# Performance work log

Hardware: AMD Instinct MI355X
Metric: run time of the kernel (lower is better)

Reference implementation:

```python
import jax, jax.numpy as jnp
import numpy as np
from jax import lax

G = 64; ELL = 0.18; VOX = ELL / G
C_VIEWS = 6; H_IMG = 256; W_IMG = 256
MAX_N = 2048; PT = 0.25; MT = 0.25; FILL = 0.45
CHUNK = 256; RADIUS_CLIP = 2.0; NEAR = 0.01


def _rotz(a):
    c, s = jnp.cos(a), jnp.sin(a)
    z = jnp.zeros_like(c); o = jnp.ones_like(c)
    return jnp.stack([jnp.stack([c, -s, z]), jnp.stack([s, c, z]), jnp.stack([z, z, o])])


def _quat_to_mat4(q):
    # faithful replication of quaternion_matrix_torch_batch (incl. its asymmetries), fp32
    eps = 4 * np.finfo(np.float32).eps
    n = jnp.sum(q * q, 1)
    qs = q * jnp.sqrt(2.0 / jnp.where(n < eps, 1.0, n))[:, None]
    o = jnp.einsum('bi,bj->bij', qs, qs)
    one = jnp.ones_like(n); zero = jnp.zeros_like(n)
    row0 = jnp.stack([1.0 - o[:, 2, 2] - o[:, 3, 3], o[:, 1, 2] - o[:, 3, 0], o[:, 1, 3] + o[:, 2, 0], zero], 1)
    row1 = jnp.stack([o[:, 1, 2] - o[:, 3, 0], one, o[:, 2, 3] - o[:, 1, 0], zero], 1)
    row2 = jnp.stack([o[:, 1, 3] - o[:, 2, 0], o[:, 2, 3] + o[:, 1, 0], 1.0 - o[:, 1, 1] - o[:, 2, 2], zero], 1)
    row3 = jnp.stack([zero, zero, zero, one], 1)
    M = jnp.stack([row0, row1, row2, row3], 1)
    return jnp.where((n < eps)[:, None, None], jnp.eye(4, dtype=q.dtype), M)


def _quat_from_mat4(m):
    m00, m01, m02 = m[:, 0, 0], m[:, 0, 1], m[:, 0, 2]
    m10, m11, m12 = m[:, 1, 0], m[:, 1, 1], m[:, 1, 2]
    m20, m21, m22 = m[:, 2, 0], m[:, 2, 1], m[:, 2, 2]
    r0 = jnp.stack([m00 - m11 - m22, m01 + m10, m02 + m20, m21 - m12], 1)
    r1 = jnp.stack([m01 + m10, m11 - m00 - m22, m12 + m21, m02 - m20], 1)
    r2 = jnp.stack([m02 + m20, m12 + m21, m22 - m00 - m11, m10 - m01], 1)
    r3 = jnp.stack([m21 - m12, m02 - m20, m10 - m01, m00 + m11 + m22], 1)
    K = jnp.stack([r0, r1, r2, r3], 1) / 3.0
    _, V = jnp.linalg.eigh(K)
    q = V[:, :, -1][:, jnp.array([3, 0, 1, 2])]
    return jnp.where(q[:, :1] < 0.0, -q, q)


def _splat(means, quats, scales, opac, colors, viewmat, K, bg):
    R3, t3 = viewmat[:3, :3], viewmat[:3, 3]
    cam = means @ R3.T + t3
    x, y, z = cam[:, 0], cam[:, 1], cam[:, 2]
    fx, fy, cx, cy = K[0, 0], K[1, 1], K[0, 2], K[1, 2]
    qn = quats / (jnp.linalg.norm(quats, axis=1, keepdims=True) + 1e-12)
    w, qx, qy, qz = qn[:, 0], qn[:, 1], qn[:, 2], qn[:, 3]
    Rq = jnp.stack([
        jnp.stack([1 - 2 * (qy * qy + qz * qz), 2 * (qx * qy - w * qz), 2 * (qx * qz + w * qy)], 1),
        jnp.stack([2 * (qx * qy + w * qz), 1 - 2 * (qx * qx + qz * qz), 2 * (qy * qz - w * qx)], 1),
        jnp.stack([2 * (qx * qz - w * qy), 2 * (qy * qz + w * qx), 1 - 2 * (qx * qx + qy * qy)], 1)], 1)
    cov3 = jnp.einsum('nij,nj,nkj->nik', Rq, scales ** 2, Rq)
    covc = jnp.einsum('ij,njk,lk->nil', R3, cov3, R3)
    rz = 1.0 / z
    zn = jnp.zeros_like(z)
    J = jnp.stack([jnp.stack([fx * rz, zn, -fx * x * rz * rz], 1),
                   jnp.stack([zn, fy * rz, -fy * y * rz * rz], 1)], 1)  # [N,2,3]
    cov2 = jnp.einsum('nij,njk,nlk->nil', J, covc, J)
    a2 = cov2[:, 0, 0] + 0.3; b2 = cov2[:, 0, 1]; c2 = cov2[:, 1, 1] + 0.3  # gsplat screen dilation
    det = a2 * c2 - b2 * b2
    det_s = jnp.where(det > 1e-12, det, 1.0)
    ca = c2 / det_s; cb = -b2 / det_s; cc = a2 / det_s  # conic
    lam = 0.5 * (a2 + c2) + jnp.sqrt(jnp.maximum(0.25 * (a2 - c2) ** 2 + b2 * b2, 1e-12))
    radius = jnp.ceil(3.0 * jnp.sqrt(lam))
    mu_x = fx * x * rz + cx; mu_y = fy * y * rz + cy
    valid = (z > NEAR) & (det > 1e-12) & (radius > RADIUS_CLIP)
    op = jnp.where(valid, opac, 0.0)
    order = jnp.argsort(z)  # front-to-back
    gac = lambda a: a[order].reshape(-1, CHUNK, *a.shape[1:])
    chunks = (gac(mu_x), gac(mu_y), gac(ca), gac(cb), gac(cc), gac(op), gac(colors))
    xs = jnp.arange(W_IMG, dtype=means.dtype) + 0.5
    ys = jnp.arange(H_IMG, dtype=means.dtype) + 0.5

    @jax.checkpoint
    def body(carry, ch):
        rgb, T = carry
        ux, uy, A, B, Cc, o_, col = ch
        dx = xs[None, None, :] - ux[:, None, None]          # [c,1,W]->[c,H,W]
        dy = ys[None, :, None] - uy[:, None, None]
        sigma = 0.5 * (A[:, None, None] * dx * dx + Cc[:, None, None] * dy * dy) + B[:, None, None] * dx * dy
        alpha = o_[:, None, None] * jnp.exp(-sigma)
        alpha = jnp.where((sigma >= 0) & (alpha >= 1.0 / 255.0), jnp.minimum(alpha, 0.999), 0.0)
        cp = jnp.cumprod(1.0 - alpha, axis=0)
        Tin = jnp.concatenate([jnp.ones_like(cp[:1]), cp[:-1]], 0)  # exclusive transmittance in chunk
        wgt = alpha * Tin * T[None]
        rgb = rgb + jnp.einsum('nhw,nc->hwc', wgt, col)
        return (rgb, T * cp[-1]), None

    init = (jnp.zeros((H_IMG, W_IMG, 3), means.dtype), jnp.ones((H_IMG, W_IMG), means.dtype))
    (rgb, T), _ = lax.scan(body, init, chunks)
    alpha_img = 1.0 - T
    rgb = jnp.clip(rgb + T[..., None] * bg, 0.0, 1.0)
    return rgb[None], alpha_img[None, :, :, None]


def _forward(mask, img, p_3d, angle, grid, Ks, viewmats, w1, b1, w2, b2, scale_param, background, view_num):
    m = mask[0]; im = img[0]
    Rz = _rotz(angle)
    # ---- shape carving: project canonical grid into all views ----
    pw = grid @ Rz.T + p_3d                                   # [V,3]
    cam = jnp.einsum('cij,vj->cvi', viewmats[:, :3, :3], pw) + viewmats[:, None, :3, 3]
    z = cam[..., 2]
    proj = jnp.einsum('cij,cvj->cvi', Ks, cam)
    u = proj[..., 0] / z; v = proj[..., 1] / z
    ui = jnp.clip(jnp.round(u).astype(jnp.int32), 0, W_IMG - 1)
    vi = jnp.clip(jnp.round(v).astype(jnp.int32), 0, H_IMG - 1)
    inb = (u >= 0) & (u < W_IMG) & (v >= 0) & (v < H_IMG) & (z > NEAR)
    cidx = jnp.arange(C_VIEWS)[:, None]
    inside = inb & (m[cidx, vi, ui] > 0.5)
    csamp = im[cidx, vi, ui]                                  # [C,V,3]
    wv = inside.astype(grid.dtype)
    frac = wv.mean(0)
    col = (wv[..., None] * csamp).sum(0) / jnp.maximum(wv.sum(0), 1.0)[:, None]
    col = jnp.where((frac >= 1.0 - 1e-6)[:, None], col, FILL)
    volume = jnp.concatenate([10.0 * frac[None] - 5.0, col.T,
                              jnp.zeros((4, grid.shape[0]), grid.dtype)], 0)  # [8, G^3] (ablation pad)
    # ---- gaussian param extraction (static top-k instead of threshold search) ----
    probs = jax.nn.sigmoid(volume[0] - MT)
    _, idx = lax.top_k(probs, MAX_N)
    feats = volume[:, idx].T                                  # [N,8]
    h = jax.nn.relu(feats @ w1 + b1)
    out = h @ w2 + b2
    quats, scl, _op, cols, dmu = jnp.split(out, [4, 7, 8, 11], axis=1)
    colors = jnp.clip(jax.nn.sigmoid(cols), 0.0, 0.99)
    scales = jnp.exp(scl + scale_param[0])
    opac = jax.nn.sigmoid(jnp.clip((probs[idx] - PT) / (1.0 - PT), 0.0, 1.0))
    means = grid[idx] + 2.0 * VOX * jnp.tanh(dmu)
    # ---- pose transform ----
    means = means @ Rz.T + p_3d
    Rz4 = jnp.eye(4, dtype=means.dtype).at[:3, :3].set(Rz)
    r = jnp.einsum('ij,bjk->bik', Rz4, _quat_to_mat4(quats))
    quats = _quat_from_mat4(r)
    return _splat(means, quats, scales, opac, colors, viewmats[view_num], Ks[view_num], background)


def setup_inputs() -> dict:
    key = jax.random.key(0)
    ks = jax.random.split(key, 6)
    mask = jax.random.uniform(ks[0], (1, C_VIEWS, H_IMG, W_IMG), jnp.float32)
    img = jax.random.uniform(ks[1], (1, C_VIEWS, H_IMG, W_IMG, 3), jnp.float32)
    p_3d = jax.random.normal(ks[2], (3,), jnp.float32) * 0.02
    angle = jax.random.uniform(ks[3], (), jnp.float32) * 2.0 * np.pi
    lin = np.linspace(-ELL / 2, ELL / 2, G, dtype=np.float32)
    gx, gy, gz = np.meshgrid(lin, lin, lin, indexing='ij')
    grid = jnp.asarray(np.stack([gx, gy, gz], -1).reshape(-1, 3))
    Kmat = np.array([[300.0, 0.0, W_IMG / 2], [0.0, 300.0, H_IMG / 2], [0.0, 0.0, 1.0]], np.float32)
    Ks = jnp.asarray(np.stack([Kmat] * C_VIEWS))
    vms = []
    up = np.array([0.0, 0.0, 1.0])
    for i in range(C_VIEWS):
        th = 2 * np.pi * i / C_VIEWS
        eye = np.array([0.8 * np.cos(th), 0.8 * np.sin(th), 0.25])
        f = -eye / np.linalg.norm(eye)
        r = np.cross(f, up); r = r / np.linalg.norm(r)
        d = np.cross(f, r)
        vm = np.eye(4, dtype=np.float32)
        vm[:3, :3] = np.stack([r, d, f]).astype(np.float32)
        vm[:3, 3] = -vm[:3, :3] @ eye.astype(np.float32)
        vms.append(vm)
    viewmats = jnp.asarray(np.stack(vms))
    w1 = jax.random.normal(ks[4], (8, 128), jnp.float32) * 0.3
    b1 = jnp.zeros((128,), jnp.float32)
    w2 = jax.random.normal(ks[5], (128, 14), jnp.float32) * 0.2
    b2 = jnp.zeros((14,), jnp.float32)
    scale_param = jnp.full((1,), -5.5, jnp.float32)
    background = jnp.ones((3,), jnp.float32)
    return dict(mask=mask, img=img, p_3d=p_3d, angle=angle, grid=grid, Ks=Ks, viewmats=viewmats,
                w1=w1, b1=b1, w2=w2, b2=b2, scale_param=scale_param, background=background, view_num=0)


def reference(mask, img, p_3d, angle, grid, Ks, viewmats, w1, b1, w2, b2, scale_param, background, view_num):
    return _forward(mask, img, p_3d, angle, grid, Ks, viewmats, w1, b1, w2, b2, scale_param, background, view_num)
```

## Files before the change

kernel.cpp:

```cpp
#include <hip/hip_runtime.h>
#include <hip/hip_bf16.h>

namespace {
constexpr int GN   = 262144;
constexpr int CV   = 6;
constexpr int HI   = 256, WI = 256;
constexpr int MAXN = 2048;
constexpr int NBLK = GN / 256;
constexpr int NSEG = 8;
constexpr float NEARZ = 0.01f;
constexpr float FILLC = 0.45f;

constexpr size_t OFF_CNT   = 0;
constexpr size_t OFF_BC    = OFF_CNT + GN;
constexpr size_t OFF_BO    = OFF_BC + 7*NBLK*4;
constexpr size_t OFF_TOT   = OFF_BO + 7*NBLK*4;
constexpr size_t OFF_SEL   = OFF_TOT + 64;
constexpr size_t OFF_SCNT  = OFF_SEL + MAXN*4;
constexpr size_t OFF_PAR   = OFF_SCNT + MAXN*4;
constexpr size_t OFF_KEY   = OFF_PAR + MAXN*12*4;
constexpr size_t OFF_RNK   = OFF_KEY + MAXN*8;
constexpr size_t OFF_SPAR  = OFF_RNK + 8*MAXN*4;
constexpr size_t OFF_PART  = OFF_SPAR + MAXN*12*4;
constexpr size_t WS_NEED   = OFF_PART + (size_t)256*NSEG*256*16;
}

__device__ __forceinline__ float sigm_(float x){ return 1.0f/(1.0f+expf(-x)); }

__global__ void k_count(const float* __restrict__ mask, const float* __restrict__ grid,
                        const float* __restrict__ p3d, const float* __restrict__ angle,
                        const float* __restrict__ Ks, const float* __restrict__ vms,
                        unsigned char* __restrict__ cnt8, int* __restrict__ bc)
{
  int p = blockIdx.x*256 + threadIdx.x;
  float a = angle[0];
  float ca = cosf(a), sa = sinf(a);
  float gx = grid[p*3+0], gy = grid[p*3+1], gz = grid[p*3+2];
  float pwx = ca*gx - sa*gy + p3d[0];
  float pwy = sa*gx + ca*gy + p3d[1];
  float pwz = gz + p3d[2];
  int count = 0;
  for (int c = 0; c < CV; ++c){
    const float* R = vms + c*16;
    float cxx = R[0]*pwx + R[1]*pwy + R[2]*pwz + R[3];
    float cyy = R[4]*pwx + R[5]*pwy + R[6]*pwz + R[7];
    float czz = R[8]*pwx + R[9]*pwy + R[10]*pwz + R[11];
    const float* K = Ks + c*9;
    float u = (K[0]*cxx + K[1]*cyy + K[2]*czz)/czz;
    float v = (K[3]*cxx + K[4]*cyy + K[5]*czz)/czz;
    bool inb = (u>=0.f)&&(u<(float)WI)&&(v>=0.f)&&(v<(float)HI)&&(czz>NEARZ);
    int ui = (int)fminf(fmaxf(rintf(u),0.f),(float)(WI-1));
    int vi = (int)fminf(fmaxf(rintf(v),0.f),(float)(HI-1));
    bool inside = inb && (mask[(c*HI+vi)*WI+ui] > 0.5f);
    count += inside ? 1 : 0;
  }
  cnt8[p] = (unsigned char)count;
  __shared__ int lh[7];
  if (threadIdx.x < 7) lh[threadIdx.x] = 0;
  __syncthreads();
  atomicAdd(&lh[6-count], 1);
  __syncthreads();
  if (threadIdx.x < 7) bc[threadIdx.x*NBLK + blockIdx.x] = lh[threadIdx.x];
}

__global__ void __launch_bounds__(1024) k_scan(const int* __restrict__ bc,
                                               int* __restrict__ bo, int* __restrict__ tot)
{
  int L = blockIdx.x;
  __shared__ int s[NBLK];
  int t = threadIdx.x;
  int v = bc[L*NBLK + t];
  s[t] = v;
  __syncthreads();
  for (int ofs = 1; ofs < NBLK; ofs <<= 1){
    int x = (t >= ofs) ? s[t-ofs] : 0;
    __syncthreads();
    s[t] += x;
    __syncthreads();
  }
  bo[L*NBLK + t] = s[t] - v;
  if (t == NBLK-1) tot[L] = s[NBLK-1];
}

__global__ void k_select(const unsigned char* __restrict__ cnt8,
                         const int* __restrict__ bo, const int* __restrict__ tot,
                         int* __restrict__ sel, int* __restrict__ scnt)
{
  int t = threadIdx.x, blk = blockIdx.x;
  int p = blk*256 + t;
  int cnt = cnt8[p];
  int L = 6 - cnt;
  int lsL = 0;
  #pragma unroll
  for (int l = 0; l < 6; ++l) if (l < L) lsL += tot[l];
  unsigned long long msk[7];
  #pragma unroll
  for (int lv = 0; lv < 7; ++lv) msk[lv] = __ballot(L == lv);
  int lane = t & 63, wv = t >> 6;
  __shared__ int wcnt[4][7];
  if (lane < 7) wcnt[wv][lane] = (int)__popcll(msk[lane]);
  __syncthreads();
  int local = (int)__popcll(msk[L] & ((1ull<<lane)-1ull));
  for (int w = 0; w < wv; ++w) local += wcnt[w][L];
  int pos = lsL + bo[L*NBLK + blk] + local;
  if (pos < MAXN){ sel[pos] = p; scnt[pos] = cnt; }
}

#define JROT(dp,dq,opq, okp1,okq1, okp2,okq2, vp0,vq0,vp1,vq1,vp2,vq2,vp3,vq3)  \
  { float apq_ = opq;                                                           \
    if (fabsf(apq_) > 1e-30f){                                                  \
      float th_ = (dq - dp)/(2.f*apq_);                                         \
      float tt_ = (th_>=0.f?1.f:-1.f)/(fabsf(th_)+sqrtf(th_*th_+1.f));          \
      float c_ = 1.f/sqrtf(tt_*tt_+1.f), s_ = tt_*c_;                           \
      dp -= tt_*apq_; dq += tt_*apq_; opq = 0.f;                                \
      float t1_=okp1, t2_=okq1; okp1 = c_*t1_ - s_*t2_; okq1 = s_*t1_ + c_*t2_; \
      t1_=okp2; t2_=okq2; okp2 = c_*t1_ - s_*t2_; okq2 = s_*t1_ + c_*t2_;       \
      t1_=vp0; t2_=vq0; vp0 = c_*t1_ - s_*t2_; vq0 = s_*t1_ + c_*t2_;           \
      t1_=vp1; t2_=vq1; vp1 = c_*t1_ - s_*t2_; vq1 = s_*t1_ + c_*t2_;           \
      t1_=vp2; t2_=vq2; vp2 = c_*t1_ - s_*t2_; vq2 = s_*t1_ + c_*t2_;           \
      t1_=vp3; t2_=vq3; vp3 = c_*t1_ - s_*t2_; vq3 = s_*t1_ + c_*t2_;           \
    } }

__global__ void __launch_bounds__(64, 1) k_mlp_params(
    const float* __restrict__ mask, const float* __restrict__ img,
    const float* __restrict__ grid, const float* __restrict__ p3d,
    const float* __restrict__ angle, const float* __restrict__ Ks,
    const float* __restrict__ vms, const float* __restrict__ w1,
    const float* __restrict__ b1, const float* __restrict__ w2,
    const float* __restrict__ b2, const float* __restrict__ scp,
    const int* __restrict__ vnp, const int* __restrict__ sel,
    const int* __restrict__ scnt, float* __restrict__ par,
    unsigned long long* __restrict__ keys)
{
  __shared__ float4 w1t[128];
  __shared__ float4 w2t[128*4];
  __shared__ float  b1s[128];
  __shared__ float  b2s[16];
  int t = threadIdx.x;
  for (int j = t; j < 128; j += 64){
    w1t[j] = make_float4(w1[j], w1[128+j], w1[256+j], w1[384+j]);
    b1s[j] = b1[j];
  }
  {
    float* w2f = (float*)w2t;
    for (int i = t; i < 2048; i += 64){
      int j = i >> 4, c = i & 15;
      w2f[i] = (c < 14) ? w2[j*14+c] : 0.f;
    }
  }
  if (t < 14) b2s[t] = b2[t];
  else if (t < 16) b2s[t] = 0.f;
  __syncthreads();
  int s = blockIdx.x*64 + t;
  int p = sel[s];
  int cnt = scnt[s];
  float a = angle[0];
  float cA = cosf(a), sA = sinf(a);
  float gx = grid[p*3+0], gy = grid[p*3+1], gz = grid[p*3+2];
  float pwx = cA*gx - sA*gy + p3d[0];
  float pwy = sA*gx + cA*gy + p3d[1];
  float pwz = gz + p3d[2];
  float sr = 0.f, sg = 0.f, sb = 0.f;
  #pragma unroll
  for (int c = 0; c < CV; ++c){
    const float* R = vms + c*16;
    float cxx = R[0]*pwx + R[1]*pwy + R[2]*pwz + R[3];
    float cyy = R[4]*pwx + R[5]*pwy + R[6]*pwz + R[7];
    float czz = R[8]*pwx + R[9]*pwy + R[10]*pwz + R[11];
    const float* K = Ks + c*9;
    float u = (K[0]*cxx + K[1]*cyy + K[2]*czz)/czz;
    float v = (K[3]*cxx + K[4]*cyy + K[5]*czz)/czz;
    bool inb = (u>=0.f)&&(u<(float)WI)&&(v>=0.f)&&(v<(float)HI)&&(czz>NEARZ);
    int ui = (int)fminf(fmaxf(rintf(u),0.f),(float)(WI-1));
    int vi = (int)fminf(fmaxf(rintf(v),0.f),(float)(HI-1));
    bool inside = inb && (mask[(c*HI+vi)*WI+ui] > 0.5f);
    if (inside){
      const float* ip = img + ((size_t)(c*HI+vi)*WI+ui)*3;
      sr += ip[0]; sg += ip[1]; sb += ip[2];
    }
  }
  float f0 = 10.f*((float)cnt/6.f) - 5.f;
  float f1, f2, f3;
  if (cnt == 6){ f1 = sr/6.f; f2 = sg/6.f; f3 = sb/6.f; }
  else { f1 = FILLC; f2 = FILLC; f3 = FILLC; }
  float o0=b2s[0],o1=b2s[1],o2=b2s[2],o3=b2s[3],o4=b2s[4],o5=b2s[5],o6=b2s[6];
  float o7=b2s[7],o8=b2s[8],o9=b2s[9],o10=b2s[10],o11=b2s[11],o12=b2s[12],o13=b2s[13];
  #pragma unroll 4
  for (int j = 0; j < 128; ++j){
    float4 wv = w1t[j];
    float hj = b1s[j] + f0*wv.x + f1*wv.y + f2*wv.z + f3*wv.w;
    hj = fmaxf(hj, 0.f);
    float4 wa = w2t[j*4+0], wb = w2t[j*4+1], wc = w2t[j*4+2], wd = w2t[j*4+3];
    o0 += hj*wa.x;  o1 += hj*wa.y;  o2 += hj*wa.z;  o3 += hj*wa.w;
    o4 += hj*wb.x;  o5 += hj*wb.y;  o6 += hj*wb.z;  o7 += hj*wb.w;
    o8 += hj*wc.x;  o9 += hj*wc.y;  o10 += hj*wc.z; o11 += hj*wc.w;
    o12 += hj*wd.x; o13 += hj*wd.y;
  }
  float q0=o0, q1=o1, q2=o2, q3=o3;
  float nq = q0*q0+q1*q1+q2*q2+q3*q3;
  float M00,M01,M02,M10,M11,M12,M20,M21,M22;
  if (nq < 4.76837158e-07f){
    M00=1.f;M01=0.f;M02=0.f;M10=0.f;M11=1.f;M12=0.f;M20=0.f;M21=0.f;M22=1.f;
  } else {
    float s2 = 2.0f/nq;
    float e11=q1*q1*s2, e22=q2*q2*s2, e33=q3*q3*s2;
    float e12=q1*q2*s2, e13=q1*q3*s2, e23=q2*q3*s2;
    float e10=q1*q0*s2, e20=q2*q0*s2, e30=q3*q0*s2;
    M00=1.f-e22-e33; M01=e12-e30; M02=e13+e20;
    M10=e12-e30;     M11=1.f;     M12=e23-e10;
    M20=e13-e20;     M21=e23+e10; M22=1.f-e11-e22;
  }
  float r00 = cA*M00 - sA*M10, r01 = cA*M01 - sA*M11, r02 = cA*M02 - sA*M12;
  float r10 = sA*M00 + cA*M10, r11 = sA*M01 + cA*M11, r12 = sA*M02 + cA*M12;
  float r20 = M20, r21 = M21, r22 = M22;
  float d0=(r00-r11-r22)/3.f, d1=(r11-r00-r22)/3.f, d2=(r22-r00-r11)/3.f, d3=(r00+r11+r22)/3.f;
  float g01=(r01+r10)/3.f, g02=(r02+r20)/3.f, g03=(r21-r12)/3.f;
  float g12=(r12+r21)/3.f, g13=(r02-r20)/3.f, g23=(r10-r01)/3.f;
  float v00=1.f,v01=0.f,v02=0.f,v03=0.f;
  float v10=0.f,v11=1.f,v12=0.f,v13=0.f;
  float v20=0.f,v21=0.f,v22=1.f,v23=0.f;
  float v30=0.f,v31=0.f,v32=0.f,v33=1.f;
  for (int sweep = 0; sweep < 7; ++sweep){
    JROT(d0,d1,g01, g02,g12, g03,g13, v00,v01, v10,v11, v20,v21, v30,v31)
    JROT(d0,d2,g02, g01,g12, g03,g23, v00,v02, v10,v12, v20,v22, v30,v32)
    JROT(d0,d3,g03, g01,g13, g02,g23, v00,v03, v10,v13, v20,v23, v30,v33)
    JROT(d1,d2,g12, g01,g02, g13,g23, v01,v02, v11,v12, v21,v22, v31,v32)
    JROT(d1,d3,g13, g01,g03, g12,g23, v01,v03, v11,v13, v21,v23, v31,v33)
    JROT(d2,d3,g23, g02,g03, g12,g13, v02,v03, v12,v13, v22,v23, v32,v33)
  }
  float bv = d0, qw = v30, qx = v00, qy = v10, qz = v20;
  if (d1 > bv){ bv = d1; qw = v31; qx = v01; qy = v11; qz = v21; }
  if (d2 > bv){ bv = d2; qw = v32; qx = v02; qy = v12; qz = v22; }
  if (d3 > bv){ bv = d3; qw = v33; qx = v03; qy = v13; qz = v23; }
  float qlen = sqrtf(qw*qw+qx*qx+qy*qy+qz*qz) + 1e-12f;
  float w = qw/qlen, x = qx/qlen, y = qy/qlen, z = qz/qlen;
  float Rq00 = 1.f-2.f*(y*y+z*z), Rq01 = 2.f*(x*y - w*z), Rq02 = 2.f*(x*z + w*y);
  float Rq10 = 2.f*(x*y + w*z), Rq11 = 1.f-2.f*(x*x+z*z), Rq12 = 2.f*(y*z - w*x);
  float Rq20 = 2.f*(x*z - w*y), Rq21 = 2.f*(y*z + w*x), Rq22 = 1.f-2.f*(x*x+y*y);
  float spv = scp[0];
  float sc0 = expf(o4+spv), sc1 = expf(o5+spv), sc2 = expf(o6+spv);
  float va = sc0*sc0, vb = sc1*sc1, vc = sc2*sc2;
  float C300 = Rq00*Rq00*va + Rq01*Rq01*vb + Rq02*Rq02*vc;
  float C301 = Rq00*Rq10*va + Rq01*Rq11*vb + Rq02*Rq12*vc;
  float C302 = Rq00*Rq20*va + Rq01*Rq21*vb + Rq02*Rq22*vc;
  float C311 = Rq10*Rq10*va + Rq11*Rq11*vb + Rq12*Rq12*vc;
  float C312 = Rq10*Rq20*va + Rq11*Rq21*vb + Rq12*Rq22*vc;
  float C322 = Rq20*Rq20*va + Rq21*Rq21*vb + Rq22*Rq22*vc;
  const float TWOVOX = (float)(2.0*(0.18/64.0));
  float mlx = gx + TWOVOX*tanhf(o11);
  float mly = gy + TWOVOX*tanhf(o12);
  float mlz = gz + TWOVOX*tanhf(o13);
  float mx = cA*mlx - sA*mly + p3d[0];
  float my = sA*mlx + cA*mly + p3d[1];
  float mz = mlz + p3d[2];
  int vn = vnp[0];
  const float* vm = vms + vn*16;
  const float* Kc = Ks + vn*9;
  float xc = vm[0]*mx + vm[1]*my + vm[2]*mz + vm[3];
  float yc = vm[4]*mx + vm[5]*my + vm[6]*mz + vm[7];
  float zc = vm[8]*mx + vm[9]*my + vm[10]*mz + vm[11];
  float R0=vm[0], R1=vm[1], R2=vm[2], R4=vm[4], R5=vm[5], R6=vm[6], R8=vm[8], R9=vm[9], R10=vm[10];
  float T00 = R0*C300 + R1*C301 + R2*C302;
  float T01 = R0*C301 + R1*C311 + R2*C312;
  float T02 = R0*C302 + R1*C312 + R2*C322;
  float T10 = R4*C300 + R5*C301 + R6*C302;
  float T11 = R4*C301 + R5*C311 + R6*C312;
  float T12 = R4*C302 + R5*C312 + R6*C322;
  float T20 = R8*C300 + R9*C301 + R10*C302;
  float T21 = R8*C301 + R9*C311 + R10*C312;
  float T22 = R8*C302 + R9*C312 + R10*C322;
  float cc00 = T00*R0 + T01*R1 + T02*R2;
  float cc01 = T00*R4 + T01*R5 + T02*R6;
  float cc02 = T00*R8 + T01*R9 + T02*R10;
  float cc11 = T10*R4 + T11*R5 + T12*R6;
  float cc12 = T10*R8 + T11*R9 + T12*R10;
  float cc22 = T20*R8 + T21*R9 + T22*R10;
  float fx = Kc[0], fy = Kc[4], cxk = Kc[2], cyk = Kc[5];
  float rz = 1.f/zc;
  float jx0 = fx*rz, jx2 = -fx*xc*rz*rz;
  float jy1 = fy*rz, jy2 = -fy*yc*rz*rz;
  float c2_00 = jx0*jx0*cc00 + 2.f*jx0*jx2*cc02 + jx2*jx2*cc22;
  float c2_01 = jx0*jy1*cc01 + jx0*jy2*cc02 + jx2*jy1*cc12 + jx2*jy2*cc22;
  float c2_11 = jy1*jy1*cc11 + 2.f*jy1*jy2*cc12 + jy2*jy2*cc22;
  float a2 = c2_00 + 0.3f, b2v = c2_01, c2 = c2_11 + 0.3f;
  float det = a2*c2 - b2v*b2v;
  float dets = (det > 1e-12f) ? det : 1.f;
  float conA = c2/dets, conB = -b2v/dets, conC = a2/dets;
  float lam = 0.5f*(a2+c2) + sqrtf(fmaxf(0.25f*(a2-c2)*(a2-c2) + b2v*b2v, 1e-12f));
  float radius = ceilf(3.f*sqrtf(lam));
  float mux = fx*xc*rz + cxk, muy = fy*yc*rz + cyk;
  bool valid = (zc > NEARZ) && (det > 1e-12f) && (radius > 2.0f);
  float prob = sigm_(10.f*((float)cnt/6.f) - 5.f - 0.25f);
  float t01 = fminf(fmaxf((prob - 0.25f)/0.75f, 0.f), 1.f);
  float opac = sigm_(t01);
  float op = valid ? opac : 0.f;
  float colr = fminf(fmaxf(sigm_(o8), 0.f), 0.99f);
  float colg = fminf(fmaxf(sigm_(o9), 0.f), 0.99f);
  float colb = fminf(fmaxf(sigm_(o10), 0.f), 0.99f);
  float tln = (op > 0.f) ? logf(255.f*op) : 0.f;
  float rxp = sqrtf(fmaxf(2.f*tln*a2, 0.f)) + 1.0f;
  float ryp = sqrtf(fmaxf(2.f*tln*c2, 0.f)) + 1.0f;
  float* pr = par + s*12;
  pr[0]=mux; pr[1]=muy; pr[2]=conA; pr[3]=conB; pr[4]=conC;
  pr[5]=op; pr[6]=colr; pr[7]=colg; pr[8]=colb; pr[9]=zc;
  pr[10] = valid ? rxp : -1e9f;
  pr[11] = valid ? ryp : -1e9f;
  unsigned int zb = __float_as_uint(zc);
  zb = (zb & 0x80000000u) ? ~zb : (zb | 0x80000000u);
  keys[s] = ((unsigned long long)zb << 11) | (unsigned long long)s;
}

__global__ void __launch_bounds__(256) k_rank(const unsigned long long* __restrict__ keys,
                                              int* __restrict__ rnk)
{
  int iblk = blockIdx.x >> 3, jblk = blockIdx.x & 7;
  __shared__ unsigned long long jk[256];
  int t = threadIdx.x;
  jk[t] = keys[jblk*256 + t];
  unsigned long long ki = keys[iblk*256 + t];
  __syncthreads();
  int cnt = 0;
  #pragma unroll 8
  for (int n = 0; n < 256; ++n) cnt += (jk[n] < ki) ? 1 : 0;
  rnk[jblk*MAXN + iblk*256 + t] = cnt;
}

__global__ void __launch_bounds__(256) k_finish(const int* __restrict__ rnk,
                                                const float* __restrict__ par,
                                                float* __restrict__ spar)
{
  int i = blockIdx.x*256 + threadIdx.x;
  int rank = 0;
  #pragma unroll
  for (int jb = 0; jb < 8; ++jb) rank += rnk[jb*MAXN + i];
  const float* src = par + i*12;
  float* dst = spar + rank*12;
  #pragma unroll
  for (int q = 0; q < 12; ++q) dst[q] = src[q];
}

__global__ void __launch_bounds__(256) k_raster_part(const float* __restrict__ spar,
                                                     float4* __restrict__ part)
{
  int raw = blockIdx.x;
  int seg = raw & (NSEG-1);
  int tilep = raw >> 3;
  int tile = (tilep*97 + seg*31) & 255;
  int tx = tile & 15, ty = tile >> 4;
  int lx = threadIdx.x & 15, ly = threadIdx.x >> 4;
  float pxc = tx*16 + lx + 0.5f, pyc = ty*16 + ly + 0.5f;
  float tileX0 = tx*16 + 0.5f, tileX1 = tx*16 + 15.5f;
  float tileY0 = ty*16 + 0.5f, tileY1 = ty*16 + 15.5f;
  __shared__ float lp[256*9];
  __shared__ int wbase[4];
  int lane = threadIdx.x & 63, wv = threadIdx.x >> 6;
  const float* gp = spar + (size_t)(seg*256 + threadIdx.x)*12;
  float mux = gp[0], muy = gp[1], op = gp[5], rx = gp[10], ry = gp[11];
  bool keep = (op > 0.f) &&
              (mux + rx >= tileX0) && (mux - rx <= tileX1) &&
              (muy + ry >= tileY0) && (muy - ry <= tileY1);
  unsigned long long m = __ballot(keep);
  if (lane == 0) wbase[wv] = (int)__popcll(m);
  __syncthreads();
  int base = 0, total = 0;
  #pragma unroll
  for (int w = 0; w < 4; ++w){ if (w < wv) base += wbase[w]; total += wbase[w]; }
  if (keep){
    int pos = base + (int)__popcll(m & ((1ull<<lane)-1ull));
    float* dst = lp + pos*9;
    dst[0]=mux; dst[1]=muy; dst[2]=gp[2]; dst[3]=gp[3]; dst[4]=gp[4];
    dst[5]=op;  dst[6]=gp[6]; dst[7]=gp[7]; dst[8]=gp[8];
  }
  __syncthreads();
  float T = 1.f, rr = 0.f, gg = 0.f, bb = 0.f;
  for (int n = 0; n < total; ++n){
    const float* g = lp + n*9;
    float dx = pxc - g[0], dy = pyc - g[1];
    float sig = 0.5f*(g[2]*dx*dx + g[4]*dy*dy) + g[3]*dx*dy;
    float alpha = g[5]*expf(-sig);
    if (sig >= 0.f && alpha >= 1.0f/255.0f){
      alpha = fminf(alpha, 0.999f);
      float wgt = alpha*T;
      rr += wgt*g[6]; gg += wgt*g[7]; bb += wgt*g[8];
      T *= (1.f - alpha);
    }
  }
  part[(size_t)(tile*NSEG + seg)*256 + threadIdx.x] = make_float4(rr, gg, bb, T);
}

__global__ void __launch_bounds__(256) k_combine(const float4* __restrict__ part,
                                                 const float* __restrict__ bg,
                                                 float* __restrict__ outp)
{
  int tile = blockIdx.x;
  int t = threadIdx.x;
  int tx = tile & 15, ty = tile >> 4;
  int px = tx*16 + (t & 15), py = ty*16 + (t >> 4);
  float rr = 0.f, gg = 0.f, bb = 0.f, T = 1.f;
  #pragma unroll
  for (int seg = 0; seg < NSEG; ++seg){
    float4 v = part[(size_t)(tile*NSEG + seg)*256 + t];
    rr += T*v.x; gg += T*v.y; bb += T*v.z; T *= v.w;
  }
  int pix = py*WI + px;
  outp[pix*3+0] = fminf(fmaxf(rr + T*bg[0], 0.f), 1.f);
  outp[pix*3+1] = fminf(fmaxf(gg + T*bg[1], 0.f), 1.f);
  outp[pix*3+2] = fminf(fmaxf(bb + T*bg[2], 0.f), 1.f);
  outp[HI*WI*3 + pix] = 1.f - T;
}

__global__ void __launch_bounds__(256) k_raster_mono(const float* __restrict__ spar,
                                                     const float* __restrict__ bg,
                                                     float* __restrict__ outp)
{
  int tile = blockIdx.x;
  int tx = tile & 15, ty = tile >> 4;
  int lx = threadIdx.x & 15, ly = threadIdx.x >> 4;
  int px = tx*16 + lx, py = ty*16 + ly;
  float pxc = px + 0.5f, pyc = py + 0.5f;
  float tileX0 = tx*16 + 0.5f, tileX1 = tx*16 + 15.5f;
  float tileY0 = ty*16 + 0.5f, tileY1 = ty*16 + 15.5f;
  float T = 1.f, rr = 0.f, gg = 0.f, bb = 0.f;
  __shared__ float lp[256*9];
  __shared__ int wbase[4];
  int lane = threadIdx.x & 63, wv = threadIdx.x >> 6;
  for (int ch = 0; ch < MAXN; ch += 256){
    const float* gp = spar + (size_t)(ch + threadIdx.x)*12;
    float mux = gp[0], muy = gp[1], op = gp[5], rx = gp[10], ry = gp[11];
    bool keep = (op > 0.f) &&
                (mux + rx >= tileX0) && (mux - rx <= tileX1) &&
                (muy + ry >= tileY0) && (muy - ry <= tileY1);
    unsigned long long m = __ballot(keep);
    int wc = (int)__popcll(m);
    __syncthreads();
    if (lane == 0) wbase[wv] = wc;
    __syncthreads();
    int base = 0, total = 0;
    #pragma unroll
    for (int w = 0; w < 4; ++w){ if (w < wv) base += wbase[w]; total += wbase[w]; }
    if (keep){
      int pos = base + (int)__popcll(m & ((1ull<<lane)-1ull));
      float* dst = lp + pos*9;
      dst[0]=mux; dst[1]=muy; dst[2]=gp[2]; dst[3]=gp[3]; dst[4]=gp[4];
      dst[5]=op;  dst[6]=gp[6]; dst[7]=gp[7]; dst[8]=gp[8];
    }
    __syncthreads();
    for (int n = 0; n < total; ++n){
      const float* g = lp + n*9;
      float dx = pxc - g[0], dy = pyc - g[1];
      float sig = 0.5f*(g[2]*dx*dx + g[4]*dy*dy) + g[3]*dx*dy;
      float alpha = g[5]*expf(-sig);
      if (sig >= 0.f && alpha >= 1.0f/255.0f){
        alpha = fminf(alpha, 0.999f);
        float wgt = alpha*T;
        rr += wgt*g[6]; gg += wgt*g[7]; bb += wgt*g[8];
        T *= (1.f - alpha);
      }
    }
  }
  int pix = py*WI + px;
  outp[pix*3+0] = fminf(fmaxf(rr + T*bg[0], 0.f), 1.f);
  outp[pix*3+1] = fminf(fmaxf(gg + T*bg[1], 0.f), 1.f);
  outp[pix*3+2] = fminf(fmaxf(bb + T*bg[2], 0.f), 1.f);
  outp[HI*WI*3 + pix] = 1.f - T;
}

extern "C" void kernel_launch(void* const* d_in, const int* in_sizes, int n_in,
                              void* d_out, int out_size, void* d_ws, size_t ws_size,
                              hipStream_t stream)
{
  const float* mask  = (const float*)d_in[0];
  const float* img   = (const float*)d_in[1];
  const float* p3d   = (const float*)d_in[2];
  const float* angle = (const float*)d_in[3];
  const float* grid  = (const float*)d_in[4];
  const float* Ks    = (const float*)d_in[5];
  const float* vms   = (const float*)d_in[6];
  const float* w1    = (const float*)d_in[7];
  const float* b1    = (const float*)d_in[8];
  const float* w2    = (const float*)d_in[9];
  const float* b2    = (const float*)d_in[10];
  const float* scp   = (const float*)d_in[11];
  const float* bg    = (const float*)d_in[12];
  const int*   vn    = (const int*)d_in[13];
  float* outp = (float*)d_out;
  char* ws = (char*)d_ws;
  unsigned char* cnt8 = (unsigned char*)(ws + OFF_CNT);
  int* bc    = (int*)(ws + OFF_BC);
  int* bo    = (int*)(ws + OFF_BO);
  int* tot   = (int*)(ws + OFF_TOT);
  int* sel   = (int*)(ws + OFF_SEL);
  int* scnt  = (int*)(ws + OFF_SCNT);
  float* par   = (float*)(ws + OFF_PAR);
  unsigned long long* keys = (unsigned long long*)(ws + OFF_KEY);
  int* rnk   = (int*)(ws + OFF_RNK);
  float* spar  = (float*)(ws + OFF_SPAR);
  float4* part = (float4*)(ws + OFF_PART);

  k_count <<<NBLK, 256, 0, stream>>>(mask, grid, p3d, angle, Ks, vms, cnt8, bc);
  k_scan  <<<7, 1024, 0, stream>>>(bc, bo, tot);
  k_select<<<NBLK, 256, 0, stream>>>(cnt8, bo, tot, sel, scnt);
  k_mlp_params<<<MAXN/64, 64, 0, stream>>>(mask, img, grid, p3d, angle, Ks, vms,
                                           w1, b1, w2, b2, scp, vn, sel, scnt, par, keys);
  k_rank  <<<64, 256, 0, stream>>>(keys, rnk);
  k_finish<<<MAXN/256, 256, 0, stream>>>(rnk, par, spar);
  if (ws_size >= WS_NEED){
    k_raster_part<<<256*NSEG, 256, 0, stream>>>(spar, part);
    k_combine    <<<256, 256, 0, stream>>>(part, bg, outp);
  } else {
    k_raster_mono<<<256, 256, 0, stream>>>(spar, bg, outp);
  }
}
```

Measured before the change: 168.2 us.

## Fold block scan into select and merge rank with scatter to cut launches

Removes the separate scan kernel. Each select block now reduces the per-block level histograms itself (row-major, 8 ints per block) to get its prefix offsets and the totals. The rank and finish kernels are merged into one sort-scatter kernel that loads all 2048 keys into shared memory and counts ranks directly. This cuts two kernel launches and their intermediate buffers, at the cost of every select block redundantly reading all 1024 histograms and each sort thread doing 2048 comparisons over only 8 blocks.

Result: slower. 194.4 us (+15.6%).

```diff
diff --git a/kernel.cpp b/kernel.cpp
--- a/kernel.cpp
+++ b/kernel.cpp
@@ -12,15 +12,12 @@
 constexpr float FILLC = 0.45f;
 
 constexpr size_t OFF_CNT   = 0;
-constexpr size_t OFF_BC    = OFF_CNT + GN;
-constexpr size_t OFF_BO    = OFF_BC + 7*NBLK*4;
-constexpr size_t OFF_TOT   = OFF_BO + 7*NBLK*4;
-constexpr size_t OFF_SEL   = OFF_TOT + 64;
+constexpr size_t OFF_BC8   = OFF_CNT + GN;
+constexpr size_t OFF_SEL   = OFF_BC8 + NBLK*8*4;
 constexpr size_t OFF_SCNT  = OFF_SEL + MAXN*4;
 constexpr size_t OFF_PAR   = OFF_SCNT + MAXN*4;
 constexpr size_t OFF_KEY   = OFF_PAR + MAXN*12*4;
-constexpr size_t OFF_RNK   = OFF_KEY + MAXN*8;
-constexpr size_t OFF_SPAR  = OFF_RNK + 8*MAXN*4;
+constexpr size_t OFF_SPAR  = OFF_KEY + MAXN*8;
 constexpr size_t OFF_PART  = OFF_SPAR + MAXN*12*4;
 constexpr size_t WS_NEED   = OFF_PART + (size_t)256*NSEG*256*16;
 }
@@ -30,7 +27,7 @@
 __global__ void k_count(const float* __restrict__ mask, const float* __restrict__ grid,
                         const float* __restrict__ p3d, const float* __restrict__ angle,
                         const float* __restrict__ Ks, const float* __restrict__ vms,
-                        unsigned char* __restrict__ cnt8, int* __restrict__ bc)
+                        unsigned char* __restrict__ cnt8, int* __restrict__ bc8)
 {
   int p = blockIdx.x*256 + threadIdx.x;
   float a = angle[0];
@@ -55,54 +52,64 @@
     count += inside ? 1 : 0;
   }
   cnt8[p] = (unsigned char)count;
-  __shared__ int lh[7];
-  if (threadIdx.x < 7) lh[threadIdx.x] = 0;
+  __shared__ int lh[8];
+  if (threadIdx.x < 8) lh[threadIdx.x] = 0;
   __syncthreads();
   atomicAdd(&lh[6-count], 1);
   __syncthreads();
-  if (threadIdx.x < 7) bc[threadIdx.x*NBLK + blockIdx.x] = lh[threadIdx.x];
-}
-
-__global__ void __launch_bounds__(1024) k_scan(const int* __restrict__ bc,
-                                               int* __restrict__ bo, int* __restrict__ tot)
-{
-  int L = blockIdx.x;
-  __shared__ int s[NBLK];
-  int t = threadIdx.x;
-  int v = bc[L*NBLK + t];
-  s[t] = v;
-  __syncthreads();
-  for (int ofs = 1; ofs < NBLK; ofs <<= 1){
-    int x = (t >= ofs) ? s[t-ofs] : 0;
-    __syncthreads();
-    s[t] += x;
-    __syncthreads();
-  }
-  bo[L*NBLK + t] = s[t] - v;
-  if (t == NBLK-1) tot[L] = s[NBLK-1];
-}
-
-__global__ void k_select(const unsigned char* __restrict__ cnt8,
-                         const int* __restrict__ bo, const int* __restrict__ tot,
-                         int* __restrict__ sel, int* __restrict__ scnt)
+  if (threadIdx.x < 8) bc8[blockIdx.x*8 + threadIdx.x] = lh[threadIdx.x];
+}
+
+__global__ void __launch_bounds__(256) k_select(const unsigned char* __restrict__ cnt8,
+                                                const int* __restrict__ bc8,
+                                                int* __restrict__ sel, int* __restrict__ scnt)
 {
   int t = threadIdx.x, blk = blockIdx.x;
+  int lane = t & 63, wv = t >> 6;
+  int accP[7], accT[7];
+  #pragma unroll
+  for (int k = 0; k < 7; ++k){ accP[k] = 0; accT[k] = 0; }
+  for (int i = t; i < NBLK; i += 256){
+    const int* row = bc8 + i*8;
+    bool pre = (i < blk);
+    #pragma unroll
+    for (int k = 0; k < 7; ++k){
+      int v = row[k];
+      accT[k] += v;
+      accP[k] += pre ? v : 0;
+    }
+  }
+  __shared__ int redP[7][4], redT[7][4];
+  #pragma unroll
+  for (int k = 0; k < 7; ++k){
+    int v = accP[k];
+    #pragma unroll
+    for (int off = 32; off > 0; off >>= 1) v += __shfl_down(v, off, 64);
+    if (lane == 0) redP[k][wv] = v;
+    int u = accT[k];
+    #pragma unroll
+    for (int off = 32; off > 0; off >>= 1) u += __shfl_down(u, off, 64);
+    if (lane == 0) redT[k][wv] = u;
+  }
+  __syncthreads();
+  __shared__ int finP[7], finT[7];
+  if (t < 7)  finP[t]   = redP[t][0] + redP[t][1] + redP[t][2] + redP[t][3];
+  else if (t >= 8 && t < 15) finT[t-8] = redT[t-8][0] + redT[t-8][1] + redT[t-8][2] + redT[t-8][3];
+  __syncthreads();
   int p = blk*256 + t;
   int cnt = cnt8[p];
   int L = 6 - cnt;
   int lsL = 0;
-  #pragma unroll
-  for (int l = 0; l < 6; ++l) if (l < L) lsL += tot[l];
+  for (int l = 0; l < L; ++l) lsL += finT[l];
   unsigned long long msk[7];
   #pragma unroll
   for (int lv = 0; lv < 7; ++lv) msk[lv] = __ballot(L == lv);
-  int lane = t & 63, wv = t >> 6;
   __shared__ int wcnt[4][7];
   if (lane < 7) wcnt[wv][lane] = (int)__popcll(msk[lane]);
   __syncthreads();
   int local = (int)__popcll(msk[L] & ((1ull<<lane)-1ull));
   for (int w = 0; w < wv; ++w) local += wcnt[w][L];
-  int pos = lsL + bo[L*NBLK + blk] + local;
+  int pos = lsL + finP[L] + local;
   if (pos < MAXN){ sel[pos] = p; scnt[pos] = cnt; }
 }
 
@@ -310,31 +317,21 @@
   keys[s] = ((unsigned long long)zb << 11) | (unsigned long long)s;
 }
 
-__global__ void __launch_bounds__(256) k_rank(const unsigned long long* __restrict__ keys,
-                                              int* __restrict__ rnk)
-{
-  int iblk = blockIdx.x >> 3, jblk = blockIdx.x & 7;
-  __shared__ unsigned long long jk[256];
+__global__ void __launch_bounds__(256) k_sortscatter(const unsigned long long* __restrict__ keys,
+                                                     const float* __restrict__ par,
+                                                     float* __restrict__ spar)
+{
+  __shared__ unsigned long long kk[MAXN];
   int t = threadIdx.x;
-  jk[t] = keys[jblk*256 + t];
-  unsigned long long ki = keys[iblk*256 + t];
-  __syncthreads();
-  int cnt = 0;
+  for (int i = t; i < MAXN; i += 256) kk[i] = keys[i];
+  int i = blockIdx.x*256 + t;
+  unsigned long long ki = keys[i];
+  __syncthreads();
+  int rank = 0;
   #pragma unroll 8
-  for (int n = 0; n < 256; ++n) cnt += (jk[n] < ki) ? 1 : 0;
-  rnk[jblk*MAXN + iblk*256 + t] = cnt;
-}
-
-__global__ void __launch_bounds__(256) k_finish(const int* __restrict__ rnk,
-                                                const float* __restrict__ par,
-                                                float* __restrict__ spar)
-{
-  int i = blockIdx.x*256 + threadIdx.x;
-  int rank = 0;
-  #pragma unroll
-  for (int jb = 0; jb < 8; ++jb) rank += rnk[jb*MAXN + i];
-  const float* src = par + i*12;
-  float* dst = spar + rank*12;
+  for (int n = 0; n < MAXN; ++n) rank += (kk[n] < ki) ? 1 : 0;
+  const float* src = par + (size_t)i*12;
+  float* dst = spar + (size_t)rank*12;
   #pragma unroll
   for (int q = 0; q < 12; ++q) dst[q] = src[q];
 }
@@ -486,24 +483,19 @@
   float* outp = (float*)d_out;
   char* ws = (char*)d_ws;
   unsigned char* cnt8 = (unsigned char*)(ws + OFF_CNT);
-  int* bc    = (int*)(ws + OFF_BC);
-  int* bo    = (int*)(ws + OFF_BO);
-  int* tot   = (int*)(ws + OFF_TOT);
+  int* bc8   = (int*)(ws + OFF_BC8);
   int* sel   = (int*)(ws + OFF_SEL);
   int* scnt  = (int*)(ws + OFF_SCNT);
   float* par   = (float*)(ws + OFF_PAR);
   unsigned long long* keys = (unsigned long long*)(ws + OFF_KEY);
-  int* rnk   = (int*)(ws + OFF_RNK);
   float* spar  = (float*)(ws + OFF_SPAR);
   float4* part = (float4*)(ws + OFF_PART);
 
-  k_count <<<NBLK, 256, 0, stream>>>(mask, grid, p3d, angle, Ks, vms, cnt8, bc);
-  k_scan  <<<7, 1024, 0, stream>>>(bc, bo, tot);
-  k_select<<<NBLK, 256, 0, stream>>>(cnt8, bo, tot, sel, scnt);
-  k_mlp_params<<<MAXN/64, 64, 0, stream>>>(mask, img, grid, p3d, angle, Ks, vms,
-                                           w1, b1, w2, b2, scp, vn, sel, scnt, par, keys);
-  k_rank  <<<64, 256, 0, stream>>>(keys, rnk);
-  k_finish<<<MAXN/256, 256, 0, stream>>>(rnk, par, spar);
+  k_count      <<<NBLK, 256, 0, stream>>>(mask, grid, p3d, angle, Ks, vms, cnt8, bc8);
+  k_select     <<<NBLK, 256, 0, stream>>>(cnt8, bc8, sel, scnt);
+  k_mlp_params <<<MAXN/64, 64, 0, stream>>>(mask, img, grid, p3d, angle, Ks, vms,
+                                            w1, b1, w2, b2, scp, vn, sel, scnt, par, keys);
+  k_sortscatter<<<MAXN/256, 256, 0, stream>>>(keys, par, spar);
   if (ws_size >= WS_NEED){
     k_raster_part<<<256*NSEG, 256, 0, stream>>>(spar, part);
     k_combine    <<<256, 256, 0, stream>>>(part, bg, outp);
```

## Fuse rank/finish and raster/combine via last-block atomic counters

Applied to the files above, without the earlier changes.

Merges the rank and scatter kernels, and the partial raster and combine kernels, using per-group atomic counters: the last block to finish a group does the follow-up work. Counters are zeroed in the count kernel, and the per-block histogram is stored block-major so each block writes one contiguous 8-int row. This removes two kernel launches and their inter-kernel gaps. In exchange it adds threadfence and atomic overhead, and the combine step now runs serialized at the tail of whichever block finishes each tile last.

Result: slower. 387.5 us (+130.3%).

```diff
diff --git a/kernel.cpp b/kernel.cpp
--- a/kernel.cpp
+++ b/kernel.cpp
@@ -12,10 +12,11 @@
 constexpr float FILLC = 0.45f;
 
 constexpr size_t OFF_CNT   = 0;
-constexpr size_t OFF_BC    = OFF_CNT + GN;
-constexpr size_t OFF_BO    = OFF_BC + 7*NBLK*4;
+constexpr size_t OFF_BC8   = OFF_CNT + GN;
+constexpr size_t OFF_BO    = OFF_BC8 + NBLK*8*4;
 constexpr size_t OFF_TOT   = OFF_BO + 7*NBLK*4;
-constexpr size_t OFF_SEL   = OFF_TOT + 64;
+constexpr size_t OFF_CTR   = OFF_TOT + 64;
+constexpr size_t OFF_SEL   = OFF_CTR + 264*4;
 constexpr size_t OFF_SCNT  = OFF_SEL + MAXN*4;
 constexpr size_t OFF_PAR   = OFF_SCNT + MAXN*4;
 constexpr size_t OFF_KEY   = OFF_PAR + MAXN*12*4;
@@ -30,8 +31,13 @@
 __global__ void k_count(const float* __restrict__ mask, const float* __restrict__ grid,
                         const float* __restrict__ p3d, const float* __restrict__ angle,
                         const float* __restrict__ Ks, const float* __restrict__ vms,
-                        unsigned char* __restrict__ cnt8, int* __restrict__ bc)
-{
+                        unsigned char* __restrict__ cnt8, int* __restrict__ bc8,
+                        int* __restrict__ ctr)
+{
+  if (blockIdx.x == 0){
+    if (threadIdx.x < 8) ctr[threadIdx.x] = 0;
+    ctr[8 + threadIdx.x] = 0;
+  }
   int p = blockIdx.x*256 + threadIdx.x;
   float a = angle[0];
   float ca = cosf(a), sa = sinf(a);
@@ -55,21 +61,21 @@
     count += inside ? 1 : 0;
   }
   cnt8[p] = (unsigned char)count;
-  __shared__ int lh[7];
-  if (threadIdx.x < 7) lh[threadIdx.x] = 0;
+  __shared__ int lh[8];
+  if (threadIdx.x < 8) lh[threadIdx.x] = 0;
   __syncthreads();
   atomicAdd(&lh[6-count], 1);
   __syncthreads();
-  if (threadIdx.x < 7) bc[threadIdx.x*NBLK + blockIdx.x] = lh[threadIdx.x];
-}
-
-__global__ void __launch_bounds__(1024) k_scan(const int* __restrict__ bc,
+  if (threadIdx.x < 8) bc8[blockIdx.x*8 + threadIdx.x] = lh[threadIdx.x];
+}
+
+__global__ void __launch_bounds__(1024) k_scan(const int* __restrict__ bc8,
                                                int* __restrict__ bo, int* __restrict__ tot)
 {
   int L = blockIdx.x;
   __shared__ int s[NBLK];
   int t = threadIdx.x;
-  int v = bc[L*NBLK + t];
+  int v = bc8[t*8 + L];
   s[t] = v;
   __syncthreads();
   for (int ofs = 1; ofs < NBLK; ofs <<= 1){
@@ -310,8 +316,10 @@
   keys[s] = ((unsigned long long)zb << 11) | (unsigned long long)s;
 }
 
-__global__ void __launch_bounds__(256) k_rank(const unsigned long long* __restrict__ keys,
-                                              int* __restrict__ rnk)
+__global__ void __launch_bounds__(256) k_rankscatter(const unsigned long long* __restrict__ keys,
+                                                     const float* __restrict__ par,
+                                                     int* __restrict__ rnk, int* __restrict__ ctr,
+                                                     float* __restrict__ spar)
 {
   int iblk = blockIdx.x >> 3, jblk = blockIdx.x & 7;
   __shared__ unsigned long long jk[256];
@@ -323,24 +331,29 @@
   #pragma unroll 8
   for (int n = 0; n < 256; ++n) cnt += (jk[n] < ki) ? 1 : 0;
   rnk[jblk*MAXN + iblk*256 + t] = cnt;
-}
-
-__global__ void __launch_bounds__(256) k_finish(const int* __restrict__ rnk,
-                                                const float* __restrict__ par,
-                                                float* __restrict__ spar)
-{
-  int i = blockIdx.x*256 + threadIdx.x;
-  int rank = 0;
-  #pragma unroll
-  for (int jb = 0; jb < 8; ++jb) rank += rnk[jb*MAXN + i];
-  const float* src = par + i*12;
-  float* dst = spar + rank*12;
-  #pragma unroll
-  for (int q = 0; q < 12; ++q) dst[q] = src[q];
+  __threadfence();
+  __syncthreads();
+  __shared__ int lastf;
+  if (t == 0) lastf = (atomicAdd(&ctr[iblk], 1) == 7) ? 1 : 0;
+  __syncthreads();
+  if (lastf){
+    __threadfence();
+    int i = iblk*256 + t;
+    int rank = 0;
+    #pragma unroll
+    for (int jb = 0; jb < 8; ++jb) rank += rnk[jb*MAXN + i];
+    const float* src = par + (size_t)i*12;
+    float* dst = spar + (size_t)rank*12;
+    #pragma unroll
+    for (int q = 0; q < 12; ++q) dst[q] = src[q];
+  }
 }
 
 __global__ void __launch_bounds__(256) k_raster_part(const float* __restrict__ spar,
-                                                     float4* __restrict__ part)
+                                                     float4* __restrict__ part,
+                                                     int* __restrict__ ctr,
+                                                     const float* __restrict__ bg,
+                                                     float* __restrict__ outp)
 {
   int raw = blockIdx.x;
   int seg = raw & (NSEG-1);
@@ -386,27 +399,27 @@
     }
   }
   part[(size_t)(tile*NSEG + seg)*256 + threadIdx.x] = make_float4(rr, gg, bb, T);
-}
-
-__global__ void __launch_bounds__(256) k_combine(const float4* __restrict__ part,
-                                                 const float* __restrict__ bg,
-                                                 float* __restrict__ outp)
-{
-  int tile = blockIdx.x;
-  int t = threadIdx.x;
-  int tx = tile & 15, ty = tile >> 4;
-  int px = tx*16 + (t & 15), py = ty*16 + (t >> 4);
-  float rr = 0.f, gg = 0.f, bb = 0.f, T = 1.f;
-  #pragma unroll
-  for (int seg = 0; seg < NSEG; ++seg){
-    float4 v = part[(size_t)(tile*NSEG + seg)*256 + t];
-    rr += T*v.x; gg += T*v.y; bb += T*v.z; T *= v.w;
-  }
-  int pix = py*WI + px;
-  outp[pix*3+0] = fminf(fmaxf(rr + T*bg[0], 0.f), 1.f);
-  outp[pix*3+1] = fminf(fmaxf(gg + T*bg[1], 0.f), 1.f);
-  outp[pix*3+2] = fminf(fmaxf(bb + T*bg[2], 0.f), 1.f);
-  outp[HI*WI*3 + pix] = 1.f - T;
+  __threadfence();
+  __syncthreads();
+  __shared__ int lastf;
+  if (threadIdx.x == 0) lastf = (atomicAdd(&ctr[8 + tile], 1) == NSEG-1) ? 1 : 0;
+  __syncthreads();
+  if (lastf){
+    __threadfence();
+    int t = threadIdx.x;
+    float rr2 = 0.f, gg2 = 0.f, bb2 = 0.f, T2 = 1.f;
+    #pragma unroll
+    for (int sg = 0; sg < NSEG; ++sg){
+      float4 v = part[(size_t)(tile*NSEG + sg)*256 + t];
+      rr2 += T2*v.x; gg2 += T2*v.y; bb2 += T2*v.z; T2 *= v.w;
+    }
+    int px = tx*16 + (t & 15), py = ty*16 + (t >> 4);
+    int pix = py*WI + px;
+    outp[pix*3+0] = fminf(fmaxf(rr2 + T2*bg[0], 0.f), 1.f);
+    outp[pix*3+1] = fminf(fmaxf(gg2 + T2*bg[1], 0.f), 1.f);
+    outp[pix*3+2] = fminf(fmaxf(bb2 + T2*bg[2], 0.f), 1.f);
+    outp[HI*WI*3 + pix] = 1.f - T2;
+  }
 }
 
 __global__ void __launch_bounds__(256) k_raster_mono(const float* __restrict__ spar,
@@ -486,9 +499,10 @@
   float* outp = (float*)d_out;
   char* ws = (char*)d_ws;
   unsigned char* cnt8 = (unsigned char*)(ws + OFF_CNT);
-  int* bc    = (int*)(ws + OFF_BC);
+  int* bc8   = (int*)(ws + OFF_BC8);
   int* bo    = (int*)(ws + OFF_BO);
   int* tot   = (int*)(ws + OFF_TOT);
+  int* ctr   = (int*)(ws + OFF_CTR);
   int* sel   = (int*)(ws + OFF_SEL);
   int* scnt  = (int*)(ws + OFF_SCNT);
   float* par   = (float*)(ws + OFF_PAR);
@@ -497,16 +511,14 @@
   float* spar  = (float*)(ws + OFF_SPAR);
   float4* part = (float4*)(ws + OFF_PART);
 
-  k_count <<<NBLK, 256, 0, stream>>>(mask, grid, p3d, angle, Ks, vms, cnt8, bc);
-  k_scan  <<<7, 1024, 0, stream>>>(bc, bo, tot);
-  k_select<<<NBLK, 256, 0, stream>>>(cnt8, bo, tot, sel, scnt);
-  k_mlp_params<<<MAXN/64, 64, 0, stream>>>(mask, img, grid, p3d, angle, Ks, vms,
-                                           w1, b1, w2, b2, scp, vn, sel, scnt, par, keys);
-  k_rank  <<<64, 256, 0, stream>>>(keys, rnk);
-  k_finish<<<MAXN/256, 256, 0, stream>>>(rnk, par, spar);
+  k_count      <<<NBLK, 256, 0, stream>>>(mask, grid, p3d, angle, Ks, vms, cnt8, bc8, ctr);
+  k_scan       <<<7, 1024, 0, stream>>>(bc8, bo, tot);
+  k_select     <<<NBLK, 256, 0, stream>>>(cnt8, bo, tot, sel, scnt);
+  k_mlp_params <<<MAXN/64, 64, 0, stream>>>(mask, img, grid, p3d, angle, Ks, vms,
+                                            w1, b1, w2, b2, scp, vn, sel, scnt, par, keys);
+  k_rankscatter<<<64, 256, 0, stream>>>(keys, par, rnk, ctr, spar);
   if (ws_size >= WS_NEED){
-    k_raster_part<<<256*NSEG, 256, 0, stream>>>(spar, part);
-    k_combine    <<<256, 256, 0, stream>>>(part, bg, outp);
+    k_raster_part<<<256*NSEG, 256, 0, stream>>>(spar, part, ctr, bg, outp);
   } else {
     k_raster_mono<<<256, 256, 0, stream>>>(spar, bg, outp);
   }
```
